# Kernel optimization log

Measured on AMD Instinct MI355X. Metric: run time of the kernel, lower is better.

## Reference

```python
import jax, jax.numpy as jnp
import numpy as np

N, H, E, K, C, M = 4096, 512, 512, 64, 128, 4  # tokens, hidden, embed, categories, children/cat, max_num_children
IN = E + H  # LSTMCell input size


def setup_inputs() -> dict:
    key = jax.random.key(0)
    ks = jax.random.split(key, 12)
    s = 0.05
    return {
        "et": jax.random.normal(ks[0], (N, H), jnp.float32),
        "x": jax.random.normal(ks[1], (N, IN), jnp.float32),
        "h": jax.random.normal(ks[2], (N, H), jnp.float32),
        "c": jax.random.normal(ks[3], (N, H), jnp.float32),
        "cat": jax.random.randint(ks[4], (N,), 0, K, jnp.int32),
        "ci": jax.random.randint(ks[5], (N,), 0, M, jnp.int32),
        # per-category prediction Linear(hidden_size -> |children(category)|)
        "W_lin": jax.random.normal(ks[6], (K, C, H), jnp.float32) * s,
        "b_lin": jax.random.normal(ks[7], (K, C), jnp.float32) * s,
        # per-child-index LSTMCell(embedding+hidden -> hidden), torch gate order i,f,g,o
        "W_ih": jax.random.normal(ks[8], (M, 4 * H, IN), jnp.float32) * s,
        "W_hh": jax.random.normal(ks[9], (M, 4 * H, H), jnp.float32) * s,
        "b_ih": jax.random.normal(ks[10], (M, 4 * H), jnp.float32) * s,
        "b_hh": jax.random.normal(ks[11], (M, 4 * H), jnp.float32) * s,
    }


def reference(et, x, h, c, cat, ci, W_lin, b_lin, W_ih, W_hh, b_ih, b_hh):
    # get_log_odds: route each token to its category's Linear (gather weights, per-token matvec)
    Wg = W_lin[cat]                                   # [N, C, H]
    log_odds = jnp.einsum('nh,nch->nc', et, Wg) + b_lin[cat]  # [N, C]

    # get_next: LSTMCell selected by child_index. Only M=4 cells, so compute all
    # cells' gates densely (efficient GEMMs) and select with a one-hot mix.
    gates_all = (jnp.einsum('ni,kgi->nkg', x, W_ih)
                 + jnp.einsum('nh,kgh->nkg', h, W_hh)
                 + (b_ih + b_hh)[None])               # [N, M, 4H]
    sel = jax.nn.one_hot(ci, M, dtype=gates_all.dtype)  # [N, M]
    gates = jnp.einsum('nkg,nk->ng', gates_all, sel)     # [N, 4H]
    i_, f_, g_, o_ = jnp.split(gates, 4, axis=-1)
    c2 = jax.nn.sigmoid(f_) * c + jax.nn.sigmoid(i_) * jnp.tanh(g_)
    h2 = jax.nn.sigmoid(o_) * jnp.tanh(c2)
    return log_odds, h2, c2
```

## Files before the change

### kernel.cpp

```cpp
#include <hip/hip_runtime.h>
#include <hip/hip_bf16.h>
#include <stdint.h>

#define NTOK 4096
#define HID  512
#define INSZ 1024
#define KIN  1536
#define KSEG 768
#define KCAT 64
#define CCH  128
#define MCELL 4
#define G4H  2048

typedef unsigned short u16;
typedef __bf16 bf16x8 __attribute__((ext_vector_type(8)));
typedef float  f32x4  __attribute__((ext_vector_type(4)));

__device__ __forceinline__ u16 f2bf(float f) {
    unsigned u = __float_as_uint(f);
    u += 0x7fffu + ((u >> 16) & 1u);
    return (u16)(u >> 16);
}
__device__ __forceinline__ float bf2f(u16 v) {
    return __uint_as_float(((unsigned)v) << 16);
}
__device__ __forceinline__ void store_bf8(u16* p, float4 a, float4 b) {
    ushort4 r0, r1;
    r0.x = f2bf(a.x); r0.y = f2bf(a.y); r0.z = f2bf(a.z); r0.w = f2bf(a.w);
    r1.x = f2bf(b.x); r1.y = f2bf(b.y); r1.z = f2bf(b.z); r1.w = f2bf(b.w);
    *reinterpret_cast<ushort4*>(p) = r0;
    *reinterpret_cast<ushort4*>(p + 4) = r1;
}
__device__ __forceinline__ void gl16(const u16* g, u16* l) {
    __builtin_amdgcn_global_load_lds((const __attribute__((address_space(1))) void*)g,
                                     (__attribute__((address_space(3))) void*)l, 16, 0, 0);
}

__global__ __launch_bounds__(1024) void build_perm(
    const int* __restrict__ ci, const int* __restrict__ cat,
    int* __restrict__ meta, int* __restrict__ perm_ci,
    int* __restrict__ inv_ci, int* __restrict__ perm_cat)
{
    __shared__ int cnt_ci[MCELL], cur_ci[MCELL];
    __shared__ int cnt_cat[KCAT], cur_cat[KCAT];
    int tid = threadIdx.x;
    if (tid < MCELL) cnt_ci[tid] = 0;
    if (tid < KCAT)  cnt_cat[tid] = 0;
    __syncthreads();
    for (int t = tid; t < NTOK; t += 1024) {
        atomicAdd(&cnt_ci[ci[t]], 1);
        atomicAdd(&cnt_cat[cat[t]], 1);
    }
    __syncthreads();
    if (tid == 0) {
        int off = 0;
        for (int m = 0; m < MCELL; ++m) {
            int p = (cnt_ci[m] + 127) & ~127;
            meta[m] = p; meta[4 + m] = off; cur_ci[m] = off; off += p;
        }
        off = 0;
        for (int i = 0; i < 128; ++i) meta[136 + i] = -1;
        for (int k = 0; k < KCAT; ++k) {
            int p = (cnt_cat[k] + 63) & ~63;
            meta[8 + k] = p; meta[72 + k] = off; cur_cat[k] = off;
            for (int i = 0; i < p / 64; ++i) meta[136 + off / 64 + i] = k;
            off += p;
        }
    }
    __syncthreads();
    for (int i = tid; i < 4608; i += 1024) perm_ci[i] = -1;
    for (int i = tid; i < 8192; i += 1024) perm_cat[i] = -1;
    __syncthreads();
    for (int t = tid; t < NTOK; t += 1024) {
        int s = atomicAdd(&cur_ci[ci[t]], 1);
        perm_ci[s] = t;
        inv_ci[t] = s;
        int sc = atomicAdd(&cur_cat[cat[t]], 1);
        perm_cat[sc] = t;
    }
}

#define CH_W  (8192 * 192)
#define CH_L  (8192 * 64)
#define CH_A  (4608 * 192)
#define CH_TOT (CH_W + CH_L + CH_A)
#define PK_BLOCKS 2048

__global__ __launch_bounds__(256) void fat_pack(
    const float* __restrict__ x, const float* __restrict__ h,
    const float* __restrict__ Wih, const float* __restrict__ Whh,
    const float* __restrict__ W_lin,
    const int* __restrict__ perm_ci,
    u16* __restrict__ A_pack, u16* __restrict__ Wb, u16* __restrict__ Wlin)
{
    for (int i = blockIdx.x * 256 + threadIdx.x; i < CH_TOT; i += PK_BLOCKS * 256) {
        if (i < CH_W) {
            int row = i / 192, cc = i - row * 192;
            int m = row >> 11, j = row & 2047;
            int c = cc * 8;
            const float* src = (c < INSZ) ? (Wih + ((size_t)m * G4H + j) * INSZ + c)
                                          : (Whh + ((size_t)m * G4H + j) * HID + (c - INSZ));
            store_bf8(Wb + (size_t)row * KIN + c,
                      *(const float4*)src, *(const float4*)(src + 4));
        } else if (i < CH_W + CH_L) {
            int i2 = i - CH_W;
            int row = i2 >> 6, cc = i2 & 63;
            const float* src = W_lin + (size_t)row * HID + cc * 8;
            store_bf8(Wlin + (size_t)row * HID + cc * 8,
                      *(const float4*)src, *(const float4*)(src + 4));
        } else {
            int i3 = i - (CH_W + CH_L);
            int row = i3 / 192, cc = i3 - row * 192;
            int c = cc * 8;
            u16* dst = A_pack + (size_t)row * KIN + c;
            int t = perm_ci[row];
            if (t < 0) {
                *reinterpret_cast<int4*>(dst) = make_int4(0, 0, 0, 0);
            } else {
                const float* src = (c < INSZ) ? (x + (size_t)t * INSZ + c)
                                              : (h + (size_t)t * HID + (c - INSZ));
                store_bf8(dst, *(const float4*)src, *(const float4*)(src + 4));
            }
        }
    }
}

__global__ __launch_bounds__(256, 4) void mega_gemm(
    const u16* __restrict__ A_pack,
    const u16* __restrict__ Wb,
    const u16* __restrict__ Wlin,
    const float* __restrict__ et,
    const float* __restrict__ b_lin,
    const int* __restrict__ meta,
    const int* __restrict__ perm_cat,
    u16* __restrict__ gates0,
    u16* __restrict__ gates1,
    float* __restrict__ out)
{
    __shared__ __align__(16) u16 As[8192];
    __shared__ __align__(16) u16 Bs[8192];
    __shared__ int sperm[64];

    int tid = threadIdx.x;
    int lane = tid & 63, wave = tid >> 6;
    int rb = tid >> 3;
    int kc = (tid & 7) ^ (rb & 7);
    int qd = lane >> 4, l15 = lane & 15;
    int rsw = l15 & 7;

    int id = blockIdx.x;
    if (id < 4608) {
        int g = id & 63;
        int r = id >> 6;
        int m = g >> 4, ct = g & 15;
        int seg = r & 1, rt = r >> 1;
        int pcnt = meta[m];
        if (rt * 128 >= pcnt) return;
        int row0 = meta[4 + m] + rt * 128;
        int k0 = seg * KSEG;

        const u16* gA[4]; const u16* gB[4];
        u16* lA[4]; u16* lB[4];
        #pragma unroll
        for (int i = 0; i < 4; ++i) {
            gA[i] = A_pack + (size_t)(row0 + i * 32 + rb) * KIN + k0 + kc * 8;
            gB[i] = Wb + ((size_t)m * G4H + ct * 128 + i * 32 + rb) * KIN + k0 + kc * 8;
            lA[i] = As + (i * 256 + wave * 64) * 8;
            lB[i] = Bs + (i * 256 + wave * 64) * 8;
        }

        int wr = wave >> 1, wc = wave & 1;

        f32x4 acc[4][4];
        #pragma unroll
        for (int i = 0; i < 4; ++i)
            #pragma unroll
            for (int j = 0; j < 4; ++j)
                acc[i][j] = (f32x4){0.f, 0.f, 0.f, 0.f};

        for (int ks = 0; ks < KSEG / 64; ++ks) {
            #pragma unroll
            for (int i = 0; i < 4; ++i) { gl16(gA[i], lA[i]); gl16(gB[i], lB[i]); }
            #pragma unroll
            for (int i = 0; i < 4; ++i) { gA[i] += 64; gB[i] += 64; }
            __syncthreads();
            #pragma unroll
            for (int ks2 = 0; ks2 < 2; ++ks2) {
                bf16x8 fa[4], fb[4];
                #pragma unroll
                for (int ti = 0; ti < 4; ++ti) {
                    int row = wr * 64 + ti * 16 + l15;
                    int ch = (ks2 * 4 + qd) ^ rsw;
                    fa[ti] = *reinterpret_cast<const bf16x8*>(&As[row * 64 + ch * 8]);
                }
                #pragma unroll
                for (int tj = 0; tj < 4; ++tj) {
                    int row = wc * 64 + tj * 16 + l15;
                    int ch = (ks2 * 4 + qd) ^ rsw;
                    fb[tj] = *reinterpret_cast<const bf16x8*>(&Bs[row * 64 + ch * 8]);
                }
                #pragma unroll
                for (int ti = 0; ti < 4; ++ti)
                    #pragma unroll
                    for (int tj = 0; tj < 4; ++tj)
                        acc[ti][tj] = __builtin_amdgcn_mfma_f32_16x16x32_bf16(fa[ti], fb[tj], acc[ti][tj], 0, 0, 0);
            }
            __syncthreads();
        }

        u16* gout = seg ? gates1 : gates0;
        #pragma unroll
        for (int ti = 0; ti < 4; ++ti) {
            #pragma unroll
            for (int tj = 0; tj < 4; ++tj) {
                int gcol = ct * 128 + wc * 64 + tj * 16 + l15;
                #pragma unroll
                for (int rr = 0; rr < 4; ++rr) {
                    int grow = row0 + wr * 64 + ti * 16 + qd * 4 + rr;
                    gout[(size_t)grow * G4H + gcol] = f2bf(acc[ti][tj][rr]);
                }
            }
        }
    } else {
        int rtl = id - 4608;
        int k = meta[136 + rtl];
        if (k < 0) return;
        int r0 = rtl * 64;

        if (tid < 64) sperm[tid] = perm_cat[r0 + tid];
        __syncthreads();

        const u16* gW[4]; u16* lW[4];
        #pragma unroll
        for (int i = 0; i < 4; ++i) {
            gW[i] = Wlin + ((size_t)k * CCH + i * 32 + rb) * HID + kc * 8;
            lW[i] = As + (i * 256 + wave * 64) * 8;
        }
        int ar = tid >> 2;
        int acp = tid & 3;
        int at = sperm[ar];
        const float* asrc = (at >= 0) ? (et + (size_t)at * HID) : nullptr;

        f32x4 acc[4][2];
        #pragma unroll
        for (int i = 0; i < 4; ++i) {
            acc[i][0] = (f32x4){0.f, 0.f, 0.f, 0.f};
            acc[i][1] = (f32x4){0.f, 0.f, 0.f, 0.f};
        }

        for (int kk = 0; kk < HID; kk += 64) {
            #pragma unroll
            for (int i = 0; i < 4; ++i) { gl16(gW[i], lW[i]); gW[i] += 64; }
            #pragma unroll
            for (int j = 0; j < 2; ++j) {
                int dch = acp * 2 + j;
                int sch = dch ^ (ar & 7);
                u16* dst = &Bs[ar * 64 + dch * 8];
                if (asrc) {
                    const float* s = asrc + kk + sch * 8;
                    store_bf8(dst, *(const float4*)s, *(const float4*)(s + 4));
                } else {
                    *reinterpret_cast<int4*>(dst) = make_int4(0, 0, 0, 0);
                }
            }
            __syncthreads();
            #pragma unroll
            for (int ks2 = 0; ks2 < 2; ++ks2) {
                bf16x8 fa[4], fb[2];
                #pragma unroll
                for (int ti = 0; ti < 4; ++ti) {
                    int row = ti * 16 + l15;
                    int ch = (ks2 * 4 + qd) ^ rsw;
                    fa[ti] = *reinterpret_cast<const bf16x8*>(&Bs[row * 64 + ch * 8]);
                }
                #pragma unroll
                for (int tj = 0; tj < 2; ++tj) {
                    int row = wave * 32 + tj * 16 + l15;
                    int ch = (ks2 * 4 + qd) ^ rsw;
                    fb[tj] = *reinterpret_cast<const bf16x8*>(&As[row * 64 + ch * 8]);
                }
                #pragma unroll
                for (int ti = 0; ti < 4; ++ti)
                    #pragma unroll
                    for (int tj = 0; tj < 2; ++tj)
                        acc[ti][tj] = __builtin_amdgcn_mfma_f32_16x16x32_bf16(fa[ti], fb[tj], acc[ti][tj], 0, 0, 0);
            }
            __syncthreads();
        }

        #pragma unroll
        for (int ti = 0; ti < 4; ++ti) {
            #pragma unroll
            for (int tj = 0; tj < 2; ++tj) {
                int n = wave * 32 + tj * 16 + l15;
                float bias = b_lin[k * CCH + n];
                #pragma unroll
                for (int rr = 0; rr < 4; ++rr) {
                    int row = ti * 16 + qd * 4 + rr;
                    int t = sperm[row];
                    if (t >= 0)
                        out[(size_t)t * CCH + n] = acc[ti][tj][rr] + bias;
                }
            }
        }
    }
}

__global__ __launch_bounds__(256) void lstm_epilogue(
    const u16* __restrict__ gates0, const u16* __restrict__ gates1,
    const int* __restrict__ meta,
    const int* __restrict__ inv_ci,
    const float* __restrict__ c,
    const float* __restrict__ b_ih,
    const float* __restrict__ b_hh,
    float* __restrict__ out)
{
    int idx = blockIdx.x * 256 + threadIdx.x;
    int t = idx >> 9;
    int hh = idx & 511;
    int s = inv_ci[t];
    int m = (s >= meta[5]) + (s >= meta[6]) + (s >= meta[7]);

    const u16* g0 = gates0 + (size_t)s * G4H;
    const u16* g1 = gates1 + (size_t)s * G4H;
    const float* bi = b_ih + (size_t)m * G4H;
    const float* bh = b_hh + (size_t)m * G4H;
    float gi = bf2f(g0[hh])        + bf2f(g1[hh])        + bi[hh]        + bh[hh];
    float gf = bf2f(g0[512 + hh])  + bf2f(g1[512 + hh])  + bi[512 + hh]  + bh[512 + hh];
    float gg = bf2f(g0[1024 + hh]) + bf2f(g1[1024 + hh]) + bi[1024 + hh] + bh[1024 + hh];
    float go = bf2f(g0[1536 + hh]) + bf2f(g1[1536 + hh]) + bi[1536 + hh] + bh[1536 + hh];

    float si = 1.f / (1.f + __expf(-gi));
    float sf = 1.f / (1.f + __expf(-gf));
    float so = 1.f / (1.f + __expf(-go));
    float ct = c[(size_t)t * HID + hh];
    float c2 = sf * ct + si * tanhf(gg);
    float h2 = so * tanhf(c2);

    const size_t o_h2 = (size_t)NTOK * CCH;
    const size_t o_c2 = o_h2 + (size_t)NTOK * HID;
    out[o_h2 + (size_t)t * HID + hh] = h2;
    out[o_c2 + (size_t)t * HID + hh] = c2;
}

extern "C" void kernel_launch(void* const* d_in, const int* in_sizes, int n_in,
                              void* d_out, int out_size, void* d_ws, size_t ws_size,
                              hipStream_t stream) {
    const float* et    = (const float*)d_in[0];
    const float* x     = (const float*)d_in[1];
    const float* h     = (const float*)d_in[2];
    const float* c     = (const float*)d_in[3];
    const int*   cat   = (const int*)d_in[4];
    const int*   ci    = (const int*)d_in[5];
    const float* W_lin = (const float*)d_in[6];
    const float* b_lin = (const float*)d_in[7];
    const float* W_ih  = (const float*)d_in[8];
    const float* W_hh  = (const float*)d_in[9];
    const float* b_ih  = (const float*)d_in[10];
    const float* b_hh  = (const float*)d_in[11];
    float* out = (float*)d_out;

    char* ws = (char*)d_ws;
    int* meta     = (int*)ws;
    int* perm_ci  = (int*)(ws + 2048);
    int* perm_cat = (int*)(ws + 20480);
    int* inv_ci   = (int*)(ws + 53248);
    u16* A_pack   = (u16*)(ws + 69632);
    u16* Wb       = (u16*)(ws + 14225408);
    u16* Wlin     = (u16*)(ws + 39391232);
    u16* gates0   = (u16*)(ws + 47779840);
    u16* gates1   = (u16*)(ws + 66654208);

    build_perm<<<1, 1024, 0, stream>>>(ci, cat, meta, perm_ci, inv_ci, perm_cat);

    fat_pack<<<PK_BLOCKS, 256, 0, stream>>>(x, h, W_ih, W_hh, W_lin, perm_ci,
                                            A_pack, Wb, Wlin);

    mega_gemm<<<4608 + 128, 256, 0, stream>>>(A_pack, Wb, Wlin, et, b_lin, meta,
                                              perm_cat, gates0, gates1, out);

    lstm_epilogue<<<(NTOK * HID) / 256, 256, 0, stream>>>(gates0, gates1, meta,
                                                          inv_ci, c, b_ih, b_hh, out);
}
```

Before: 236.6 us.

## Enlarge LSTM GEMM row tile to 256 for more B-operand reuse

The LSTM gate GEMM tile grows from 128x128 to 256x128. Each wave now computes a 128x64 sub-tile with 8x4 MFMA accumulators, and per-cell row padding rises to 256. The workspace layout, the A_pack row count and the grid size are adjusted to match. The goal is to halve redundant weight-tile loads and raise MFMA work per LDS load. The cost is more padding rows, more registers, fewer blocks (launch bounds drop to 2 waves per SIMD) and worse load balance.

```diff
diff --git a/kernel.cpp b/kernel.cpp
--- a/kernel.cpp
+++ b/kernel.cpp
@@ -11,6 +11,7 @@
 #define CCH  128
 #define MCELL 4
 #define G4H  2048
+#define AROWS 5120
 
 typedef unsigned short u16;
 typedef __bf16 bf16x8 __attribute__((ext_vector_type(8)));
@@ -55,7 +56,7 @@
     if (tid == 0) {
         int off = 0;
         for (int m = 0; m < MCELL; ++m) {
-            int p = (cnt_ci[m] + 127) & ~127;
+            int p = (cnt_ci[m] + 255) & ~255;
             meta[m] = p; meta[4 + m] = off; cur_ci[m] = off; off += p;
         }
         off = 0;
@@ -68,7 +69,7 @@
         }
     }
     __syncthreads();
-    for (int i = tid; i < 4608; i += 1024) perm_ci[i] = -1;
+    for (int i = tid; i < AROWS; i += 1024) perm_ci[i] = -1;
     for (int i = tid; i < 8192; i += 1024) perm_cat[i] = -1;
     __syncthreads();
     for (int t = tid; t < NTOK; t += 1024) {
@@ -82,7 +83,7 @@
 
 #define CH_W  (8192 * 192)
 #define CH_L  (8192 * 64)
-#define CH_A  (4608 * 192)
+#define CH_A  (AROWS * 192)
 #define CH_TOT (CH_W + CH_L + CH_A)
 #define PK_BLOCKS 2048
 
@@ -125,7 +126,7 @@
     }
 }
 
-__global__ __launch_bounds__(256, 4) void mega_gemm(
+__global__ __launch_bounds__(256, 2) void mega_gemm(
     const u16* __restrict__ A_pack,
     const u16* __restrict__ Wb,
     const u16* __restrict__ Wlin,
@@ -137,98 +138,103 @@
     u16* __restrict__ gates1,
     float* __restrict__ out)
 {
-    __shared__ __align__(16) u16 As[8192];
+    __shared__ __align__(16) u16 As[16384];
     __shared__ __align__(16) u16 Bs[8192];
     __shared__ int sperm[64];
 
     int tid = threadIdx.x;
     int lane = tid & 63, wave = tid >> 6;
-    int rb = tid >> 3;
-    int kc = (tid & 7) ^ (rb & 7);
     int qd = lane >> 4, l15 = lane & 15;
     int rsw = l15 & 7;
 
     int id = blockIdx.x;
-    if (id < 4608) {
+    if (id < 1280) {
         int g = id & 63;
         int r = id >> 6;
         int m = g >> 4, ct = g & 15;
         int seg = r & 1, rt = r >> 1;
         int pcnt = meta[m];
-        if (rt * 128 >= pcnt) return;
-        int row0 = meta[4 + m] + rt * 128;
+        if (rt * 256 >= pcnt) return;
+        int row0 = meta[4 + m] + rt * 256;
         int k0 = seg * KSEG;
 
-        const u16* gA[4]; const u16* gB[4];
-        u16* lA[4]; u16* lB[4];
-        #pragma unroll
-        for (int i = 0; i < 4; ++i) {
-            gA[i] = A_pack + (size_t)(row0 + i * 32 + rb) * KIN + k0 + kc * 8;
-            gB[i] = Wb + ((size_t)m * G4H + ct * 128 + i * 32 + rb) * KIN + k0 + kc * 8;
-            lA[i] = As + (i * 256 + wave * 64) * 8;
-            lB[i] = Bs + (i * 256 + wave * 64) * 8;
-        }
-
-        int wr = wave >> 1, wc = wave & 1;
-
-        f32x4 acc[4][4];
-        #pragma unroll
-        for (int i = 0; i < 4; ++i)
+        const u16* gA[8]; const u16* gB[4];
+        u16* lA[8]; u16* lB[4];
+        #pragma unroll
+        for (int j = 0; j < 8; ++j) {
+            int q = j * 256 + wave * 64 + lane;
+            int row = q >> 3, kc = (q & 7) ^ (row & 7);
+            gA[j] = A_pack + (size_t)(row0 + row) * KIN + k0 + kc * 8;
+            lA[j] = As + q * 8;
+        }
+        #pragma unroll
+        for (int j = 0; j < 4; ++j) {
+            int q = j * 256 + wave * 64 + lane;
+            int row = q >> 3, kc = (q & 7) ^ (row & 7);
+            gB[j] = Wb + ((size_t)m * G4H + ct * 128 + row) * KIN + k0 + kc * 8;
+            lB[j] = Bs + q * 8;
+        }
+
+        int wm = wave >> 1, wn = wave & 1;
+
+        f32x4 acc[8][4];
+        #pragma unroll
+        for (int i = 0; i < 8; ++i)
             #pragma unroll
             for (int j = 0; j < 4; ++j)
                 acc[i][j] = (f32x4){0.f, 0.f, 0.f, 0.f};
 
         for (int ks = 0; ks < KSEG / 64; ++ks) {
             #pragma unroll
-            for (int i = 0; i < 4; ++i) { gl16(gA[i], lA[i]); gl16(gB[i], lB[i]); }
-            #pragma unroll
-            for (int i = 0; i < 4; ++i) { gA[i] += 64; gB[i] += 64; }
+            for (int j = 0; j < 8; ++j) { gl16(gA[j], lA[j]); gA[j] += 64; }
+            #pragma unroll
+            for (int j = 0; j < 4; ++j) { gl16(gB[j], lB[j]); gB[j] += 64; }
             __syncthreads();
             #pragma unroll
             for (int ks2 = 0; ks2 < 2; ++ks2) {
-                bf16x8 fa[4], fb[4];
-                #pragma unroll
-                for (int ti = 0; ti < 4; ++ti) {
-                    int row = wr * 64 + ti * 16 + l15;
-                    int ch = (ks2 * 4 + qd) ^ rsw;
-                    fa[ti] = *reinterpret_cast<const bf16x8*>(&As[row * 64 + ch * 8]);
-                }
+                int ch = (ks2 * 4 + qd) ^ rsw;
+                bf16x8 fb[4];
                 #pragma unroll
                 for (int tj = 0; tj < 4; ++tj) {
-                    int row = wc * 64 + tj * 16 + l15;
-                    int ch = (ks2 * 4 + qd) ^ rsw;
+                    int row = wn * 64 + tj * 16 + l15;
                     fb[tj] = *reinterpret_cast<const bf16x8*>(&Bs[row * 64 + ch * 8]);
                 }
                 #pragma unroll
-                for (int ti = 0; ti < 4; ++ti)
+                for (int ti = 0; ti < 8; ++ti) {
+                    int row = wm * 128 + ti * 16 + l15;
+                    bf16x8 fa = *reinterpret_cast<const bf16x8*>(&As[row * 64 + ch * 8]);
                     #pragma unroll
                     for (int tj = 0; tj < 4; ++tj)
-                        acc[ti][tj] = __builtin_amdgcn_mfma_f32_16x16x32_bf16(fa[ti], fb[tj], acc[ti][tj], 0, 0, 0);
+                        acc[ti][tj] = __builtin_amdgcn_mfma_f32_16x16x32_bf16(fa, fb[tj], acc[ti][tj], 0, 0, 0);
+                }
             }
             __syncthreads();
         }
 
         u16* gout = seg ? gates1 : gates0;
         #pragma unroll
-        for (int ti = 0; ti < 4; ++ti) {
+        for (int ti = 0; ti < 8; ++ti) {
             #pragma unroll
             for (int tj = 0; tj < 4; ++tj) {
-                int gcol = ct * 128 + wc * 64 + tj * 16 + l15;
+                int gcol = ct * 128 + wn * 64 + tj * 16 + l15;
                 #pragma unroll
                 for (int rr = 0; rr < 4; ++rr) {
-                    int grow = row0 + wr * 64 + ti * 16 + qd * 4 + rr;
+                    int grow = row0 + wm * 128 + ti * 16 + qd * 4 + rr;
                     gout[(size_t)grow * G4H + gcol] = f2bf(acc[ti][tj][rr]);
                 }
             }
         }
     } else {
-        int rtl = id - 4608;
+        int rtl = id - 1280;
         int k = meta[136 + rtl];
         if (k < 0) return;
         int r0 = rtl * 64;
 
         if (tid < 64) sperm[tid] = perm_cat[r0 + tid];
         __syncthreads();
+
+        int rb = tid >> 3;
+        int kc = (tid & 7) ^ (rb & 7);
 
         const u16* gW[4]; u16* lW[4];
         #pragma unroll
@@ -266,19 +272,14 @@
             __syncthreads();
             #pragma unroll
             for (int ks2 = 0; ks2 < 2; ++ks2) {
+                int ch = (ks2 * 4 + qd) ^ rsw;
                 bf16x8 fa[4], fb[2];
                 #pragma unroll
-                for (int ti = 0; ti < 4; ++ti) {
-                    int row = ti * 16 + l15;
-                    int ch = (ks2 * 4 + qd) ^ rsw;
-                    fa[ti] = *reinterpret_cast<const bf16x8*>(&Bs[row * 64 + ch * 8]);
-                }
-                #pragma unroll
-                for (int tj = 0; tj < 2; ++tj) {
-                    int row = wave * 32 + tj * 16 + l15;
-                    int ch = (ks2 * 4 + qd) ^ rsw;
-                    fb[tj] = *reinterpret_cast<const bf16x8*>(&As[row * 64 + ch * 8]);
-                }
+                for (int ti = 0; ti < 4; ++ti)
+                    fa[ti] = *reinterpret_cast<const bf16x8*>(&Bs[(ti * 16 + l15) * 64 + ch * 8]);
+                #pragma unroll
+                for (int tj = 0; tj < 2; ++tj)
+                    fb[tj] = *reinterpret_cast<const bf16x8*>(&As[(wave * 32 + tj * 16 + l15) * 64 + ch * 8]);
                 #pragma unroll
                 for (int ti = 0; ti < 4; ++ti)
                     #pragma unroll
@@ -363,20 +364,20 @@
     char* ws = (char*)d_ws;
     int* meta     = (int*)ws;
     int* perm_ci  = (int*)(ws + 2048);
-    int* perm_cat = (int*)(ws + 20480);
-    int* inv_ci   = (int*)(ws + 53248);
-    u16* A_pack   = (u16*)(ws + 69632);
-    u16* Wb       = (u16*)(ws + 14225408);
-    u16* Wlin     = (u16*)(ws + 39391232);
-    u16* gates0   = (u16*)(ws + 47779840);
-    u16* gates1   = (u16*)(ws + 66654208);
+    int* perm_cat = (int*)(ws + 22528);
+    int* inv_ci   = (int*)(ws + 55296);
+    u16* A_pack   = (u16*)(ws + 71680);
+    u16* Wb       = (u16*)(ws + 15800320);
+    u16* Wlin     = (u16*)(ws + 40966144);
+    u16* gates0   = (u16*)(ws + 49354752);
+    u16* gates1   = (u16*)(ws + 70326272);
 
     build_perm<<<1, 1024, 0, stream>>>(ci, cat, meta, perm_ci, inv_ci, perm_cat);
 
     fat_pack<<<PK_BLOCKS, 256, 0, stream>>>(x, h, W_ih, W_hh, W_lin, perm_ci,
                                             A_pack, Wb, Wlin);
 
-    mega_gemm<<<4608 + 128, 256, 0, stream>>>(A_pack, Wb, Wlin, et, b_lin, meta,
+    mega_gemm<<<1280 + 128, 256, 0, stream>>>(A_pack, Wb, Wlin, et, b_lin, meta,
                                               perm_cat, gates0, gates1, out);
 
     lstm_epilogue<<<(NTOK * HID) / 256, 256, 0, stream>>>(gates0, gates1, meta,
```

Result: no change. 236.1 us (-0.2%).
